# Kernel optimization log

Hardware: AMD Instinct MI355X
Metric: run time of the kernel (lower is better)

The kernel has to match this reference:

```python
import jax, jax.numpy as jnp
import numpy as np

D_MODEL = 1024
N_HEADS = 16
HEAD_DIM = D_MODEL // N_HEADS
D_FF = 4096
BATCH = 4
SEQ = 2048
LN_EPS = 1e-5


def layer_norm(x, g, b):
    mu = jnp.mean(x, axis=-1, keepdims=True)
    var = jnp.mean(jnp.square(x - mu), axis=-1, keepdims=True)
    return (x - mu) * jax.lax.rsqrt(var + LN_EPS) * g + b


def setup_inputs() -> dict:
    key = jax.random.key(0)
    ks = jax.random.split(key, 8)
    s = 0.02
    x = jax.random.normal(ks[0], (BATCH, SEQ, D_MODEL), jnp.float32)
    mask = jnp.triu(jnp.ones((SEQ, SEQ), dtype=bool), k=1)  # True = masked
    return {
        "x": x,
        "ln1_g": jnp.ones((D_MODEL,), jnp.float32),
        "ln1_b": jnp.zeros((D_MODEL,), jnp.float32),
        "qkv_w": jax.random.normal(ks[1], (3 * D_MODEL, D_MODEL), jnp.float32) * s,
        "qkv_b": jnp.zeros((3 * D_MODEL,), jnp.float32),
        "out_w": jax.random.normal(ks[2], (D_MODEL, D_MODEL), jnp.float32) * s,
        "out_b": jnp.zeros((D_MODEL,), jnp.float32),
        "ln2_g": jnp.ones((D_MODEL,), jnp.float32),
        "ln2_b": jnp.zeros((D_MODEL,), jnp.float32),
        "fc1_w": jax.random.normal(ks[3], (D_FF, D_MODEL), jnp.float32) * s,
        "fc1_b": jnp.zeros((D_FF,), jnp.float32),
        "fc2_w": jax.random.normal(ks[4], (D_MODEL, D_FF), jnp.float32) * s,
        "fc2_b": jnp.zeros((D_MODEL,), jnp.float32),
        "mask": mask,
    }


def reference(x, ln1_g, ln1_b, qkv_w, qkv_b, out_w, out_b,
              ln2_g, ln2_b, fc1_w, fc1_b, fc2_w, fc2_b, mask):
    b, s, _ = x.shape
    # --- pre-norm attention ---
    h = layer_norm(x, ln1_g, ln1_b)
    qkv = h @ qkv_w.T + qkv_b                       # [b, s, 3*D]
    qkv = qkv.reshape(b, s, 3, N_HEADS, HEAD_DIM)
    q, k, v = (jnp.moveaxis(qkv[:, :, i], 2, 1) for i in range(3))  # [b, H, s, hd]
    scale = HEAD_DIM ** -0.5
    attn = jnp.einsum('bhqd,bhkd->bhqk', q, k) * scale
    attn = jnp.where(mask, -jnp.inf, attn)
    attn = jax.nn.softmax(attn, axis=-1)
    o = jnp.einsum('bhqk,bhkd->bhqd', attn, v)      # [b, H, s, hd]
    o = jnp.moveaxis(o, 1, 2).reshape(b, s, D_MODEL)
    x = x + (o @ out_w.T + out_b)
    # --- pre-norm FFN ---
    h = layer_norm(x, ln2_g, ln2_b)
    h = jax.nn.gelu(h @ fc1_w.T + fc1_b, approximate=False)
    x = x + (h @ fc2_w.T + fc2_b)
    return x
```

## Files before the change

### kernel.cpp

```cpp
#include <hip/hip_runtime.h>
#include <math.h>

using u16 = unsigned short;
typedef __attribute__((ext_vector_type(8))) short short8;
typedef __attribute__((ext_vector_type(4))) float f32x4;
typedef __attribute__((ext_vector_type(16))) float f32x16;
typedef __attribute__((ext_vector_type(4))) u16 u16x4;

#define DEV __device__ __forceinline__

DEV u16 f2bf(float f) {
    unsigned u = __float_as_uint(f);
    u += 0x7fffu + ((u >> 16) & 1u);
    return (u16)(u >> 16);
}
DEV float bf2f(u16 h) { return __uint_as_float(((unsigned)h) << 16); }

DEV short8 ld16(const u16* p) { return *reinterpret_cast<const short8*>(p); }

DEV float gelu_f(float x) {
    const float u = x * (0.7978845608f + 0.0356774081f * x * x);
    const float e = __builtin_amdgcn_exp2f(u * 2.885390082f);
    const float t = 1.f - 2.f * __builtin_amdgcn_rcpf(e + 1.f);
    return 0.5f * x * (1.f + t);
}

DEV unsigned pk2(float a, float b) {
    unsigned r;
    asm("v_cvt_pk_bf16_f32 %0, %1, %2" : "=v"(r) : "v"(a), "v"(b));
    return r;
}

#define GLL16(gp, lp)                                                          \
    __builtin_amdgcn_global_load_lds(                                          \
        (const __attribute__((address_space(1))) void*)(gp),                   \
        (__attribute__((address_space(3))) void*)(lp), 16, 0, 0)

#define VMC(n) asm volatile("s_waitcnt vmcnt(" #n ")" ::: "memory")
#define LGKM0() asm volatile("s_waitcnt lgkmcnt(0)" ::: "memory")

__global__ void cvt_f32_bf16(const float* __restrict__ in, u16* __restrict__ out, int n4) {
    int i = blockIdx.x * 256 + threadIdx.x;
    if (i >= n4) return;
    float4 v = reinterpret_cast<const float4*>(in)[i];
    u16x4 o;
    o.x = f2bf(v.x); o.y = f2bf(v.y); o.z = f2bf(v.z); o.w = f2bf(v.w);
    reinterpret_cast<u16x4*>(out)[i] = o;
}

__global__ __launch_bounds__(256) void ln_bf16(const float* __restrict__ x,
                                               const float* __restrict__ gm,
                                               const float* __restrict__ bt,
                                               u16* __restrict__ out) {
    const int row = blockIdx.x, tid = threadIdx.x;
    const float4 v = reinterpret_cast<const float4*>(x + (long)row * 1024)[tid];
    float s  = v.x + v.y + v.z + v.w;
    float sq = v.x * v.x + v.y * v.y + v.z * v.z + v.w * v.w;
#pragma unroll
    for (int off = 1; off <= 32; off <<= 1) {
        s  += __shfl_xor(s, off);
        sq += __shfl_xor(sq, off);
    }
    __shared__ float ss[4], ssq[4];
    const int wave = tid >> 6, lane = tid & 63;
    if (lane == 0) { ss[wave] = s; ssq[wave] = sq; }
    __syncthreads();
    s  = ss[0] + ss[1] + ss[2] + ss[3];
    sq = ssq[0] + ssq[1] + ssq[2] + ssq[3];
    const float mu   = s * (1.f / 1024.f);
    const float var  = sq * (1.f / 1024.f) - mu * mu;
    const float rstd = rsqrtf(var + 1e-5f);
    const float4 g4 = reinterpret_cast<const float4*>(gm)[tid];
    const float4 b4 = reinterpret_cast<const float4*>(bt)[tid];
    u16x4 o;
    o.x = f2bf((v.x - mu) * rstd * g4.x + b4.x);
    o.y = f2bf((v.y - mu) * rstd * g4.y + b4.y);
    o.z = f2bf((v.z - mu) * rstd * g4.z + b4.z);
    o.w = f2bf((v.w - mu) * rstd * g4.w + b4.w);
    reinterpret_cast<u16x4*>(out + (long)row * 1024)[tid] = o;
}

#define TS(c, r) ((c) * 128 + (((((r) >> 3) ^ ((c) & 15))) << 3) + ((r) & 7))

template <int EPI>
__global__ __launch_bounds__(256, 4) void gemm_bt(
    const u16* __restrict__ A, const u16* __restrict__ B,
    const float* __restrict__ bias, const float* res, float* outf,
    u16* __restrict__ outb, u16* __restrict__ Qb, u16* __restrict__ Kb,
    u16* __restrict__ Vtb, int M, int N, int K, int ldk) {
    __shared__ u16 shpool[16384];

    const int tid = threadIdx.x;
    const int wave = tid >> 6, lane = tid & 63;
    const int lo = lane & 15, g = lane >> 4;
    const int wr = wave >> 1, wc = wave & 1;

    const int nwg = gridDim.x, chunk = nwg >> 3;
    const int wgid = (blockIdx.x & 7) * chunk + (blockIdx.x >> 3);
    const int nSmCol = N >> 10;
    const int s = wgid >> 6, w6 = wgid & 63;
    const int bm = (s / nSmCol) * 8 + (w6 >> 3);
    const int bn = (s % nSmCol) * 8 + (w6 & 7);
    const int row0 = bm * 128, col0 = bn * 128;

    const int lrow = lane >> 2;
    const int lg   = (lane & 3) ^ ((lane >> 3) & 3);
    const u16* Ag = A + (long)(row0 + wave * 16 + lrow) * ldk + lg * 8;
    const u16* Bg = B + (long)(col0 + wave * 16 + lrow) * ldk + lg * 8;

#define STAGE(tb, kt) do {                                                     \
        u16* Al = shpool + (tb) * 8192 + wave * 512;                           \
        u16* Bl = Al + 4096;                                                   \
        GLL16(Ag + (long)(kt) * 32, Al);                                       \
        GLL16(Ag + 64 * (long)ldk + (long)(kt) * 32, Al + 2048);               \
        GLL16(Bg + (long)(kt) * 32, Bl);                                       \
        GLL16(Bg + 64 * (long)ldk + (long)(kt) * 32, Bl + 2048);               \
    } while (0)

    const int agp = g ^ ((lo >> 1) & 3);
    f32x4 acc[4][4] = {};

    STAGE(0, 0);
    STAGE(1, 1);

    const int T = K >> 5;
    for (int t = 0; t < T; ++t) {
        const int cur = t & 1;
        if (t + 2 < T) { VMC(4); } else { VMC(0); }
        __builtin_amdgcn_s_barrier();
        const u16* As = shpool + cur * 8192;
        const u16* Bs = As + 4096;
        short8 af[4], bfr[4];
#pragma unroll
        for (int m = 0; m < 4; ++m)
            af[m] = ld16(&As[(wr * 64 + m * 16 + lo) * 32 + agp * 8]);
#pragma unroll
        for (int n = 0; n < 4; ++n)
            bfr[n] = ld16(&Bs[(wc * 64 + n * 16 + lo) * 32 + agp * 8]);
        LGKM0();
        __builtin_amdgcn_s_barrier();
        if (t + 2 < T) STAGE(cur, t + 2);
#pragma unroll
        for (int m = 0; m < 4; ++m)
#pragma unroll
            for (int n = 0; n < 4; ++n)
                acc[m][n] = __builtin_amdgcn_mfma_f32_16x16x32_bf16(
                    bfr[n], af[m], acc[m][n], 0, 0, 0);
    }
#undef STAGE

    if constexpr (EPI == 3) {
        if (col0 >= 2048) {
            __syncthreads();
#pragma unroll
            for (int n = 0; n < 4; ++n) {
                const int cb = wc * 64 + n * 16 + g * 4;
                const float4 b4 = *reinterpret_cast<const float4*>(&bias[col0 + cb]);
#pragma unroll
                for (int m = 0; m < 4; ++m) {
                    const int rl = wr * 64 + m * 16 + lo;
                    shpool[TS(cb + 0, rl)] = f2bf(acc[m][n][0] + b4.x);
                    shpool[TS(cb + 1, rl)] = f2bf(acc[m][n][1] + b4.y);
                    shpool[TS(cb + 2, rl)] = f2bf(acc[m][n][2] + b4.z);
                    shpool[TS(cb + 3, rl)] = f2bf(acc[m][n][3] + b4.w);
                }
            }
            __syncthreads();
            const int c = tid >> 1, hlf = tid & 1;
            const int dcol = (col0 - 2048) + c;
            const int head = dcol >> 6, d = dcol & 63;
            const int bb = row0 >> 11;
            u16* dst = Vtb + ((long)(bb * 16 + head) * 64 + d) * 2048 +
                       (row0 & 2047) + hlf * 64;
            const u16* srcb = shpool + c * 128;
#pragma unroll
            for (int i = 0; i < 8; ++i) {
                const int pc = (hlf * 8 + i) ^ (c & 15);
                *reinterpret_cast<short8*>(dst + i * 8) =
                    *reinterpret_cast<const short8*>(srcb + pc * 8);
            }
            return;
        }
    }
#pragma unroll
    for (int n = 0; n < 4; ++n) {
        const int cb = col0 + wc * 64 + n * 16 + g * 4;
        const float4 b4 = *reinterpret_cast<const float4*>(&bias[cb]);
#pragma unroll
        for (int m = 0; m < 4; ++m) {
            const int r = row0 + wr * 64 + m * 16 + lo;
            const float v0 = acc[m][n][0] + b4.x;
            const float v1 = acc[m][n][1] + b4.y;
            const float v2 = acc[m][n][2] + b4.z;
            const float v3 = acc[m][n][3] + b4.w;
            if constexpr (EPI == 0) {
                u16x4 o = {f2bf(v0), f2bf(v1), f2bf(v2), f2bf(v3)};
                *reinterpret_cast<u16x4*>(&outb[(long)r * N + cb]) = o;
            } else if constexpr (EPI == 1) {
                u16x4 o = {f2bf(gelu_f(v0)), f2bf(gelu_f(v1)),
                           f2bf(gelu_f(v2)), f2bf(gelu_f(v3))};
                *reinterpret_cast<u16x4*>(&outb[(long)r * N + cb]) = o;
            } else if constexpr (EPI == 2) {
                const float4 rr = *reinterpret_cast<const float4*>(&res[(long)r * N + cb]);
                float4 o = {rr.x + v0, rr.y + v1, rr.z + v2, rr.w + v3};
                *reinterpret_cast<float4*>(&outf[(long)r * N + cb]) = o;
            } else {
                const int part = cb >> 10, cc = cb & 1023;
                const int head = cc >> 6, d = cc & 63;
                const int bb = r >> 11, srow = r & 2047;
                const int bh = bb * 16 + head;
                const float qs = (part == 0) ? 0.18033688f : 1.0f;
                u16x4 o = {f2bf(v0 * qs), f2bf(v1 * qs), f2bf(v2 * qs), f2bf(v3 * qs)};
                u16* base = (part == 0) ? Qb : Kb;
                *reinterpret_cast<u16x4*>(&base[((long)bh * 2048 + srow) * 64 + d]) = o;
            }
        }
    }
}

__global__ __launch_bounds__(256) void attn_fwd32(
    const u16* __restrict__ Q, const u16* __restrict__ K,
    const u16* __restrict__ Vt, u16* __restrict__ O) {
    __shared__ u16 kvl[2][8192];
    const int bh = blockIdx.x;
    const int strip = 15 - blockIdx.y;
    const int wave = threadIdx.x >> 6, lane = threadIdx.x & 63;
    const int lq = lane & 31, hi = lane >> 5;
    const int qw = strip * 128 + wave * 32;

    const u16* Kg = K + (long)bh * 2048 * 64;
    const u16* Vg = Vt + (long)bh * 64 * 2048;
    const int bb = bh >> 4, h = bh & 15;
    const u16* Qp = Q + ((long)bh * 2048 + qw) * 64;

    const int srow = wave * 8 + (lane >> 3);
    const int sc   = (lane & 7) ^ (srow & 7);

#define ASTAGE(b, kt) do {                                                     \
        const long kvb = (long)(kt) * 64;                                      \
        GLL16(Kg + (kvb + srow) * 64 + sc * 8,        &kvl[b][wave * 512]);    \
        GLL16(Kg + (kvb + 32 + srow) * 64 + sc * 8,   &kvl[b][2048 + wave * 512]); \
        GLL16(Vg + (long)srow * 2048 + kvb + sc * 8,  &kvl[b][4096 + wave * 512]); \
        GLL16(Vg + (long)(32 + srow) * 2048 + kvb + sc * 8,                    \
              &kvl[b][6144 + wave * 512]);                                     \
    } while (0)

    short8 qf[4];
#pragma unroll
    for (int ks = 0; ks < 4; ++ks)
        qf[ks] = ld16(Qp + lq * 64 + ks * 16 + hi * 8);

    f32x16 o0 = {}, o1 = {};
    float m = -1e30f, l = 0.f;
    const int q_abs = qw + lq;
    const int my_end = qw + 32;
    const int T = 2 * (strip + 1);
    const int swp = lq & 7;

    ASTAGE(0, 0);
    ASTAGE(1, 1);

    for (int t = 0; t < T; ++t) {
        const int cur = t & 1;
        const int kv0 = t * 64;
        if (t + 1 < T) { VMC(4); } else { VMC(0); }
        __builtin_amdgcn_s_barrier();
        const bool active = (kv0 < my_end);
        f32x16 s0 = {}, s1 = {};
        short8 vf0[4], vf1[4];
        if (active) {
            const u16* Kb = &kvl[cur][0];
            __builtin_amdgcn_s_setprio(1);
#pragma unroll
            for (int ks = 0; ks < 4; ++ks)
                s0 = __builtin_amdgcn_mfma_f32_32x32x16_bf16(
                    ld16(Kb + lq * 64 + ((ks * 2 + hi) ^ swp) * 8), qf[ks], s0, 0, 0, 0);
#pragma unroll
            for (int ks = 0; ks < 4; ++ks)
                s1 = __builtin_amdgcn_mfma_f32_32x32x16_bf16(
                    ld16(Kb + 2048 + lq * 64 + ((ks * 2 + hi) ^ swp) * 8), qf[ks], s1, 0, 0, 0);
            __builtin_amdgcn_s_setprio(0);
            const u16* Vb = &kvl[cur][4096];
#pragma unroll
            for (int c = 0; c < 4; ++c) {
                vf0[c] = ld16(Vb + lq * 64 + ((c * 2 + hi) ^ swp) * 8);
                vf1[c] = ld16(Vb + 2048 + lq * 64 + ((c * 2 + hi) ^ swp) * 8);
            }
        }
        LGKM0();
        __builtin_amdgcn_s_barrier();
        if (t + 2 < T) ASTAGE(cur, t + 2);
        if (active) {
            float mt = -1e30f;
            if (kv0 + 64 >= my_end) {
#pragma unroll
                for (int r = 0; r < 16; ++r) {
                    const int kv = kv0 + (r & 3) + 8 * (r >> 2) + 4 * hi;
                    if (kv > q_abs) s0[r] = -1e30f;
                    mt = fmaxf(mt, s0[r]);
                    if (kv + 32 > q_abs) s1[r] = -1e30f;
                    mt = fmaxf(mt, s1[r]);
                }
            } else {
#pragma unroll
                for (int r = 0; r < 16; ++r)
                    mt = fmaxf(mt, fmaxf(s0[r], s1[r]));
            }
            mt = fmaxf(mt, __shfl_xor(mt, 32));

            if (!__all(mt <= m + 11.5f)) {
                const float mn = fmaxf(m, mt);
                const float corr = __builtin_amdgcn_exp2f(m - mn);
                m = mn;
                l *= corr;
                o0 *= corr; o1 *= corr;
            }
            float ps = 0.f;
#pragma unroll
            for (int r = 0; r < 16; ++r) {
                s0[r] = __builtin_amdgcn_exp2f(s0[r] - m); ps += s0[r];
                s1[r] = __builtin_amdgcn_exp2f(s1[r] - m); ps += s1[r];
            }
            l += ps;

            short8 pf[4];
#pragma unroll
            for (int c = 0; c < 4; ++c) {
                const f32x16& src = (c >> 1) ? s1 : s0;
                const int b = (c & 1) * 8;
                const unsigned A0 = pk2(src[b + 0], src[b + 1]);
                const unsigned A1 = pk2(src[b + 2], src[b + 3]);
                const unsigned B0 = pk2(src[b + 4], src[b + 5]);
                const unsigned B1 = pk2(src[b + 6], src[b + 7]);
                const unsigned S0 = hi ? A0 : B0;
                const unsigned S1 = hi ? A1 : B1;
                const unsigned R0 = (unsigned)__shfl_xor((int)S0, 32);
                const unsigned R1 = (unsigned)__shfl_xor((int)S1, 32);
                union { unsigned u[4]; short8 v; } fr;
                fr.u[0] = hi ? R0 : A0;
                fr.u[1] = hi ? R1 : A1;
                fr.u[2] = hi ? B0 : R0;
                fr.u[3] = hi ? B1 : R1;
                pf[c] = fr.v;
            }

            __builtin_amdgcn_s_setprio(1);
#pragma unroll
            for (int c = 0; c < 4; ++c) {
                o0 = __builtin_amdgcn_mfma_f32_32x32x16_bf16(
                    vf0[c], pf[c], o0, 0, 0, 0);
                o1 = __builtin_amdgcn_mfma_f32_32x32x16_bf16(
                    vf1[c], pf[c], o1, 0, 0, 0);
            }
            __builtin_amdgcn_s_setprio(0);
        }
    }
#undef ASTAGE

    l += __shfl_xor(l, 32);
    const float inv = 1.f / l;
    u16* Orow = O + ((long)(bb * 2048 + qw + lq)) * 1024 + h * 64;
#pragma unroll
    for (int k4 = 0; k4 < 4; ++k4) {
        u16x4 w0, w1;
#pragma unroll
        for (int j = 0; j < 4; ++j) {
            w0[j] = f2bf(o0[k4 * 4 + j] * inv);
            w1[j] = f2bf(o1[k4 * 4 + j] * inv);
        }
        *reinterpret_cast<u16x4*>(Orow + 8 * k4 + 4 * hi)      = w0;
        *reinterpret_cast<u16x4*>(Orow + 32 + 8 * k4 + 4 * hi) = w1;
    }
}

extern "C" void kernel_launch(void* const* d_in, const int* in_sizes, int n_in,
                              void* d_out, int out_size, void* d_ws, size_t ws_size,
                              hipStream_t stream) {
    const float* x      = (const float*)d_in[0];
    const float* ln1_g  = (const float*)d_in[1];
    const float* ln1_b  = (const float*)d_in[2];
    const float* qkv_w  = (const float*)d_in[3];
    const float* qkv_b  = (const float*)d_in[4];
    const float* out_w  = (const float*)d_in[5];
    const float* out_b  = (const float*)d_in[6];
    const float* ln2_g  = (const float*)d_in[7];
    const float* ln2_b  = (const float*)d_in[8];
    const float* fc1_w  = (const float*)d_in[9];
    const float* fc1_b  = (const float*)d_in[10];
    const float* fc2_w  = (const float*)d_in[11];
    const float* fc2_b  = (const float*)d_in[12];
    float* out = (float*)d_out;

    const size_t MB = 1024ull * 1024ull;
    if (ws_size < 120 * MB) return;
    char* ws = (char*)d_ws;
    u16* wqkv = (u16*)(ws + 0);
    u16* wout = (u16*)(ws + 6 * MB);
    u16* wfc1 = (u16*)(ws + 8 * MB);
    u16* wfc2 = (u16*)(ws + 16 * MB);
    u16* hbuf = (u16*)(ws + 24 * MB);
    u16* obuf = (u16*)(ws + 40 * MB);
    u16* Qb   = (u16*)(ws + 56 * MB);
    u16* Kb   = (u16*)(ws + 72 * MB);
    u16* Vtb  = (u16*)(ws + 88 * MB);
    u16* gbuf = (u16*)(ws + 56 * MB);

    cvt_f32_bf16<<<3072, 256, 0, stream>>>(qkv_w, wqkv, 3072 * 1024 / 4);
    cvt_f32_bf16<<<1024, 256, 0, stream>>>(out_w, wout, 1024 * 1024 / 4);
    cvt_f32_bf16<<<4096, 256, 0, stream>>>(fc1_w, wfc1, 4096 * 1024 / 4);
    cvt_f32_bf16<<<4096, 256, 0, stream>>>(fc2_w, wfc2, 1024 * 4096 / 4);

    ln_bf16<<<8192, 256, 0, stream>>>(x, ln1_g, ln1_b, hbuf);
    gemm_bt<3><<<dim3(1536), 256, 0, stream>>>(hbuf, wqkv, qkv_b, nullptr,
                                               nullptr, nullptr, Qb, Kb, Vtb,
                                               8192, 3072, 1024, 1024);
    attn_fwd32<<<dim3(64, 16), 256, 0, stream>>>(Qb, Kb, Vtb, obuf);
    gemm_bt<2><<<dim3(512), 256, 0, stream>>>(obuf, wout, out_b, x, out,
                                              nullptr, nullptr, nullptr, nullptr,
                                              8192, 1024, 1024, 1024);
    ln_bf16<<<8192, 256, 0, stream>>>(out, ln2_g, ln2_b, hbuf);
    gemm_bt<1><<<dim3(2048), 256, 0, stream>>>(hbuf, wfc1, fc1_b, nullptr,
                                               nullptr, gbuf, nullptr, nullptr,
                                               nullptr, 8192, 4096, 1024, 1024);
    gemm_bt<2><<<dim3(512), 256, 0, stream>>>(gbuf, wfc2, fc2_b, out, out,
                                              nullptr, nullptr, nullptr, nullptr,
                                              8192, 1024, 4096, 4096);
}
```

Measured before the change: 378.7 us.

## Add BK=64 GEMM variant for N=1024 GEMMs and LDS-staged coalesced epilogues

```diff
diff --git a/kernel.cpp b/kernel.cpp
--- a/kernel.cpp
+++ b/kernel.cpp
@@ -81,14 +81,16 @@
 }
 
 #define TS(c, r) ((c) * 128 + (((((r) >> 3) ^ ((c) & 15))) << 3) + ((r) & 7))
-
-template <int EPI>
-__global__ __launch_bounds__(256, 4) void gemm_bt(
+#define CS(r, ck) ((r) * 128 + ((((ck) ^ ((r) & 15))) << 3))
+
+template <int EPI, int BK>
+__global__ __launch_bounds__(256, (BK == 32) ? 4 : 2) void gemm_bt(
     const u16* __restrict__ A, const u16* __restrict__ B,
     const float* __restrict__ bias, const float* res, float* outf,
     u16* __restrict__ outb, u16* __restrict__ Qb, u16* __restrict__ Kb,
     u16* __restrict__ Vtb, int M, int N, int K, int ldk) {
-    __shared__ u16 shpool[16384];
+    constexpr int BUFU = (BK == 32) ? 8192 : 16384;
+    __shared__ u16 shpool[2 * BUFU];
 
     const int tid = threadIdx.x;
     const int wave = tid >> 6, lane = tid & 63;
@@ -103,54 +105,130 @@
     const int bn = (s % nSmCol) * 8 + (w6 & 7);
     const int row0 = bm * 128, col0 = bn * 128;
 
-    const int lrow = lane >> 2;
-    const int lg   = (lane & 3) ^ ((lane >> 3) & 3);
-    const u16* Ag = A + (long)(row0 + wave * 16 + lrow) * ldk + lg * 8;
-    const u16* Bg = B + (long)(col0 + wave * 16 + lrow) * ldk + lg * 8;
-
-#define STAGE(tb, kt) do {                                                     \
-        u16* Al = shpool + (tb) * 8192 + wave * 512;                           \
-        u16* Bl = Al + 4096;                                                   \
-        GLL16(Ag + (long)(kt) * 32, Al);                                       \
-        GLL16(Ag + 64 * (long)ldk + (long)(kt) * 32, Al + 2048);               \
-        GLL16(Bg + (long)(kt) * 32, Bl);                                       \
-        GLL16(Bg + 64 * (long)ldk + (long)(kt) * 32, Bl + 2048);               \
-    } while (0)
-
-    const int agp = g ^ ((lo >> 1) & 3);
+    const u16 *Ag, *Bg;
+    if constexpr (BK == 32) {
+        const int lrow = lane >> 2;
+        const int lg   = (lane & 3) ^ ((lane >> 3) & 3);
+        Ag = A + (long)(row0 + wave * 16 + lrow) * ldk + lg * 8;
+        Bg = B + (long)(col0 + wave * 16 + lrow) * ldk + lg * 8;
+    } else {
+        const int lg = (lane & 7) ^ ((lane >> 3) & 7);
+        Ag = A + (long)(row0 + wave * 32 + (lane >> 3)) * ldk + lg * 8;
+        Bg = B + (long)(col0 + wave * 32 + (lane >> 3)) * ldk + lg * 8;
+    }
+
+    auto STAGE = [&](int tb, int kt) {
+        if constexpr (BK == 32) {
+            u16* Al = shpool + tb * 8192 + wave * 512;
+            u16* Bl = Al + 4096;
+            GLL16(Ag + (long)kt * 32, Al);
+            GLL16(Ag + 64 * (long)ldk + (long)kt * 32, Al + 2048);
+            GLL16(Bg + (long)kt * 32, Bl);
+            GLL16(Bg + 64 * (long)ldk + (long)kt * 32, Bl + 2048);
+        } else {
+            u16* Al = shpool + tb * 16384 + wave * 2048;
+            u16* Bl = Al + 8192;
+            GLL16(Ag + (long)kt * 64,                  Al);
+            GLL16(Ag + (long)kt * 64 +  8 * (long)ldk, Al + 512);
+            GLL16(Ag + (long)kt * 64 + 16 * (long)ldk, Al + 1024);
+            GLL16(Ag + (long)kt * 64 + 24 * (long)ldk, Al + 1536);
+            GLL16(Bg + (long)kt * 64,                  Bl);
+            GLL16(Bg + (long)kt * 64 +  8 * (long)ldk, Bl + 512);
+            GLL16(Bg + (long)kt * 64 + 16 * (long)ldk, Bl + 1024);
+            GLL16(Bg + (long)kt * 64 + 24 * (long)ldk, Bl + 1536);
+        }
+    };
+
     f32x4 acc[4][4] = {};
 
     STAGE(0, 0);
     STAGE(1, 1);
 
-    const int T = K >> 5;
+    const int T = K / BK;
     for (int t = 0; t < T; ++t) {
         const int cur = t & 1;
-        if (t + 2 < T) { VMC(4); } else { VMC(0); }
+        if (t + 1 < T) {
+            if constexpr (BK == 32) { VMC(4); } else { VMC(8); }
+        } else { VMC(0); }
         __builtin_amdgcn_s_barrier();
-        const u16* As = shpool + cur * 8192;
-        const u16* Bs = As + 4096;
-        short8 af[4], bfr[4];
-#pragma unroll
-        for (int m = 0; m < 4; ++m)
-            af[m] = ld16(&As[(wr * 64 + m * 16 + lo) * 32 + agp * 8]);
-#pragma unroll
-        for (int n = 0; n < 4; ++n)
-            bfr[n] = ld16(&Bs[(wc * 64 + n * 16 + lo) * 32 + agp * 8]);
-        LGKM0();
-        __builtin_amdgcn_s_barrier();
-        if (t + 2 < T) STAGE(cur, t + 2);
-#pragma unroll
-        for (int m = 0; m < 4; ++m)
+        const u16* As = shpool + cur * BUFU;
+        const u16* Bs = As + BUFU / 2;
+        if constexpr (BK == 32) {
+            short8 af[4], bfr[4];
+            const int agp = g ^ ((lo >> 1) & 3);
+#pragma unroll
+            for (int m = 0; m < 4; ++m)
+                af[m] = ld16(&As[(wr * 64 + m * 16 + lo) * 32 + agp * 8]);
 #pragma unroll
             for (int n = 0; n < 4; ++n)
-                acc[m][n] = __builtin_amdgcn_mfma_f32_16x16x32_bf16(
-                    bfr[n], af[m], acc[m][n], 0, 0, 0);
-    }
-#undef STAGE
+                bfr[n] = ld16(&Bs[(wc * 64 + n * 16 + lo) * 32 + agp * 8]);
+            LGKM0();
+            __builtin_amdgcn_s_barrier();
+            if (t + 2 < T) STAGE(cur, t + 2);
+#pragma unroll
+            for (int m = 0; m < 4; ++m)
+#pragma unroll
+                for (int n = 0; n < 4; ++n)
+                    acc[m][n] = __builtin_amdgcn_mfma_f32_16x16x32_bf16(
+                        bfr[n], af[m], acc[m][n], 0, 0, 0);
+        } else {
+            short8 af[2][4], bfr[2][4];
+#pragma unroll
+            for (int ks = 0; ks < 2; ++ks) {
+                const int ch = ((ks * 4 + g) ^ (lo & 7)) * 8;
+#pragma unroll
+                for (int m = 0; m < 4; ++m)
+                    af[ks][m] = ld16(&As[(wr * 64 + m * 16 + lo) * 64 + ch]);
+#pragma unroll
+                for (int n = 0; n < 4; ++n)
+                    bfr[ks][n] = ld16(&Bs[(wc * 64 + n * 16 + lo) * 64 + ch]);
+            }
+            LGKM0();
+            __builtin_amdgcn_s_barrier();
+            if (t + 2 < T) STAGE(cur, t + 2);
+#pragma unroll
+            for (int ks = 0; ks < 2; ++ks)
+#pragma unroll
+                for (int m = 0; m < 4; ++m)
+#pragma unroll
+                    for (int n = 0; n < 4; ++n)
+                        acc[m][n] = __builtin_amdgcn_mfma_f32_16x16x32_bf16(
+                            bfr[ks][n], af[ks][m], acc[m][n], 0, 0, 0);
+        }
+    }
+
+    if constexpr (EPI == 1) {
+#pragma unroll
+        for (int n = 0; n < 4; ++n) {
+            const int cb = col0 + wc * 64 + n * 16 + g * 4;
+            const float4 b4 = *reinterpret_cast<const float4*>(&bias[cb]);
+            const int ch = wc * 8 + n * 2 + (g >> 1);
+#pragma unroll
+            for (int m = 0; m < 4; ++m) {
+                const int r = wr * 64 + m * 16 + lo;
+                u16x4 o = {f2bf(gelu_f(acc[m][n][0] + b4.x)),
+                           f2bf(gelu_f(acc[m][n][1] + b4.y)),
+                           f2bf(gelu_f(acc[m][n][2] + b4.z)),
+                           f2bf(gelu_f(acc[m][n][3] + b4.w))};
+                *reinterpret_cast<u16x4*>(&shpool[CS(r, ch) + (g & 1) * 4]) = o;
+            }
+        }
+        __syncthreads();
+        const int row = tid >> 1, hl = tid & 1;
+        u16* drow = outb + (long)(row0 + row) * N + col0 + hl * 64;
+        const int rk = row & 15;
+#pragma unroll
+        for (int i = 0; i < 8; ++i) {
+            const int ck = hl * 8 + i;
+            *reinterpret_cast<short8*>(drow + i * 8) =
+                *reinterpret_cast<const short8*>(&shpool[row * 128 + ((ck ^ rk) << 3)]);
+        }
+        return;
+    }
 
     if constexpr (EPI == 3) {
-        if (col0 >= 2048) {
+        const int part = col0 >> 10;
+        if (part == 2) {
             __syncthreads();
 #pragma unroll
             for (int n = 0; n < 4; ++n) {
@@ -181,7 +259,40 @@
             }
             return;
         }
-    }
+        const float qs = (part == 0) ? 0.18033688f : 1.0f;
+#pragma unroll
+        for (int n = 0; n < 4; ++n) {
+            const int cb = col0 + wc * 64 + n * 16 + g * 4;
+            const float4 b4 = *reinterpret_cast<const float4*>(&bias[cb]);
+            const int ch = wc * 8 + n * 2 + (g >> 1);
+#pragma unroll
+            for (int m = 0; m < 4; ++m) {
+                const int r = wr * 64 + m * 16 + lo;
+                u16x4 o = {f2bf((acc[m][n][0] + b4.x) * qs),
+                           f2bf((acc[m][n][1] + b4.y) * qs),
+                           f2bf((acc[m][n][2] + b4.z) * qs),
+                           f2bf((acc[m][n][3] + b4.w) * qs)};
+                *reinterpret_cast<u16x4*>(&shpool[CS(r, ch) + (g & 1) * 4]) = o;
+            }
+        }
+        __syncthreads();
+        const int row = tid >> 1, hl = tid & 1;
+        const int headbase = (col0 & 1023) >> 6;
+        const int head = headbase + hl;
+        const int bb = row0 >> 11;
+        const int srow = (row0 & 2047) + row;
+        u16* drow = (part == 0 ? Qb : Kb) +
+                    ((long)(bb * 16 + head) * 2048 + srow) * 64;
+        const int rk = row & 15;
+#pragma unroll
+        for (int i = 0; i < 8; ++i) {
+            const int ck = hl * 8 + i;
+            *reinterpret_cast<short8*>(drow + i * 8) =
+                *reinterpret_cast<const short8*>(&shpool[row * 128 + ((ck ^ rk) << 3)]);
+        }
+        return;
+    }
+
 #pragma unroll
     for (int n = 0; n < 4; ++n) {
         const int cb = col0 + wc * 64 + n * 16 + g * 4;
@@ -189,31 +300,10 @@
 #pragma unroll
         for (int m = 0; m < 4; ++m) {
             const int r = row0 + wr * 64 + m * 16 + lo;
-            const float v0 = acc[m][n][0] + b4.x;
-            const float v1 = acc[m][n][1] + b4.y;
-            const float v2 = acc[m][n][2] + b4.z;
-            const float v3 = acc[m][n][3] + b4.w;
-            if constexpr (EPI == 0) {
-                u16x4 o = {f2bf(v0), f2bf(v1), f2bf(v2), f2bf(v3)};
-                *reinterpret_cast<u16x4*>(&outb[(long)r * N + cb]) = o;
-            } else if constexpr (EPI == 1) {
-                u16x4 o = {f2bf(gelu_f(v0)), f2bf(gelu_f(v1)),
-                           f2bf(gelu_f(v2)), f2bf(gelu_f(v3))};
-                *reinterpret_cast<u16x4*>(&outb[(long)r * N + cb]) = o;
-            } else if constexpr (EPI == 2) {
-                const float4 rr = *reinterpret_cast<const float4*>(&res[(long)r * N + cb]);
-                float4 o = {rr.x + v0, rr.y + v1, rr.z + v2, rr.w + v3};
-                *reinterpret_cast<float4*>(&outf[(long)r * N + cb]) = o;
-            } else {
-                const int part = cb >> 10, cc = cb & 1023;
-                const int head = cc >> 6, d = cc & 63;
-                const int bb = r >> 11, srow = r & 2047;
-                const int bh = bb * 16 + head;
-                const float qs = (part == 0) ? 0.18033688f : 1.0f;
-                u16x4 o = {f2bf(v0 * qs), f2bf(v1 * qs), f2bf(v2 * qs), f2bf(v3 * qs)};
-                u16* base = (part == 0) ? Qb : Kb;
-                *reinterpret_cast<u16x4*>(&base[((long)bh * 2048 + srow) * 64 + d]) = o;
-            }
+            const float4 rr = *reinterpret_cast<const float4*>(&res[(long)r * N + cb]);
+            float4 o = {rr.x + acc[m][n][0] + b4.x, rr.y + acc[m][n][1] + b4.y,
+                        rr.z + acc[m][n][2] + b4.z, rr.w + acc[m][n][3] + b4.w};
+            *reinterpret_cast<float4*>(&outf[(long)r * N + cb]) = o;
         }
     }
 }
@@ -411,18 +501,18 @@
     cvt_f32_bf16<<<4096, 256, 0, stream>>>(fc2_w, wfc2, 1024 * 4096 / 4);
 
     ln_bf16<<<8192, 256, 0, stream>>>(x, ln1_g, ln1_b, hbuf);
-    gemm_bt<3><<<dim3(1536), 256, 0, stream>>>(hbuf, wqkv, qkv_b, nullptr,
-                                               nullptr, nullptr, Qb, Kb, Vtb,
-                                               8192, 3072, 1024, 1024);
+    gemm_bt<3, 32><<<dim3(1536), 256, 0, stream>>>(hbuf, wqkv, qkv_b, nullptr,
+                                                   nullptr, nullptr, Qb, Kb, Vtb,
+                                                   8192, 3072, 1024, 1024);
     attn_fwd32<<<dim3(64, 16), 256, 0, stream>>>(Qb, Kb, Vtb, obuf);
-    gemm_bt<2><<<dim3(512), 256, 0, stream>>>(obuf, wout, out_b, x, out,
-                                              nullptr, nullptr, nullptr, nullptr,
-                                              8192, 1024, 1024, 1024);
+    gemm_bt<2, 64><<<dim3(512), 256, 0, stream>>>(obuf, wout, out_b, x, out,
+                                                  nullptr, nullptr, nullptr, nullptr,
+                                                  8192, 1024, 1024, 1024);
     ln_bf16<<<8192, 256, 0, stream>>>(out, ln2_g, ln2_b, hbuf);
-    gemm_bt<1><<<dim3(2048), 256, 0, stream>>>(hbuf, wfc1, fc1_b, nullptr,
-                                               nullptr, gbuf, nullptr, nullptr,
-                                               nullptr, 8192, 4096, 1024, 1024);
-    gemm_bt<2><<<dim3(512), 256, 0, stream>>>(gbuf, wfc2, fc2_b, out, out,
-                                              nullptr, nullptr, nullptr, nullptr,
-                                              8192, 1024, 4096, 4096);
-}
+    gemm_bt<1, 32><<<dim3(2048), 256, 0, stream>>>(hbuf, wfc1, fc1_b, nullptr,
+                                                   nullptr, gbuf, nullptr, nullptr,
+                                                   nullptr, 8192, 4096, 1024, 1024);
+    gemm_bt<2, 64><<<dim3(512), 256, 0, stream>>>(gbuf, wfc2, fc2_b, out, out,
+                                                  nullptr, nullptr, nullptr, nullptr,
+                                                  8192, 1024, 4096, 4096);
+}
```

Result: faster. 371.1 us (-2.0%).
